# Kernel optimization log

Hardware: AMD Instinct MI355X
Metric: run time of the kernel (lower is better)

## Reference

```python
import jax, jax.numpy as jnp
import numpy as np

N_HEADS = 12

def setup_inputs() -> dict:
    key = jax.random.key(0)
    k1, k2, k3 = jax.random.split(key, 3)
    B, S, W = 8, 1024, 768
    x = jax.random.normal(k1, (B, S, W), dtype=jnp.float32)
    w_qkv = jax.random.normal(k2, (W, 3 * W), dtype=jnp.float32) * (W ** -0.5)
    w_out = jax.random.normal(k3, (W, W), dtype=jnp.float32) * (W ** -0.5)
    return {"x": x, "w_qkv": w_qkv, "w_out": w_out}

def reference(x, w_qkv, w_out):
    B, S, W = x.shape
    H = N_HEADS
    D = W // H  # head_width
    scale = W ** -0.5  # NOTE: source scales by width**-0.5, not head_width**-0.5
    qkv = x @ w_qkv  # [B, S, 3W]
    q, k, v = jnp.split(qkv, 3, axis=2)
    q = q.reshape(B, S, H, D)
    k = k.reshape(B, S, H, D)
    # attn_score: [B, i, j, n]
    attn_score = jnp.einsum('binh,bjnh->bijn', q, k) * scale
    attn_weight = jax.nn.softmax(attn_score, axis=2)
    # NOTE: source uses K (not V) here — faithful reproduction of the bug.
    out = jnp.einsum('bijn,bjnh->binh', attn_weight, k)
    out = out.reshape(B, S, W)
    return out @ w_out  # dropout is identity in eval
```

## Files before the change

kernel.cpp:

```cpp
#include <hip/hip_runtime.h>

#define US unsigned short

typedef __bf16 bf16x8 __attribute__((ext_vector_type(8)));
typedef short s16x8 __attribute__((ext_vector_type(8)));
typedef short s16x4 __attribute__((ext_vector_type(4)));
typedef float f32x4 __attribute__((ext_vector_type(4)));

static __device__ __forceinline__ US f2bf(float f) {
  union { float f; unsigned u; } x; x.f = f;
  unsigned r = x.u + 0x7fffu + ((x.u >> 16) & 1u);
  return (US)(r >> 16);
}

static __device__ __forceinline__ unsigned packbf(float lo, float hi) {
  return (unsigned)f2bf(lo) | ((unsigned)f2bf(hi) << 16);
}

static __device__ __forceinline__ void gload16(const US* g, US* l) {
  __builtin_amdgcn_global_load_lds(
      (const __attribute__((address_space(1))) void*)g,
      (__attribute__((address_space(3))) void*)l, 16, 0, 0);
}

__global__ __launch_bounds__(256) void cast_f32_bf16(
    const float* __restrict__ src, US* __restrict__ dst) {
  int i = blockIdx.x * 256 + threadIdx.x;
  const float4* s = (const float4*)src + (size_t)i * 2;
  float4 a = s[0], b = s[1];
  s16x8 w;
  w[0] = (short)f2bf(a.x); w[1] = (short)f2bf(a.y);
  w[2] = (short)f2bf(a.z); w[3] = (short)f2bf(a.w);
  w[4] = (short)f2bf(b.x); w[5] = (short)f2bf(b.y);
  w[6] = (short)f2bf(b.z); w[7] = (short)f2bf(b.w);
  *(s16x8*)(dst + (size_t)i * 8) = w;
}

__global__ __launch_bounds__(256) void transpose_cast_k(
    const float* __restrict__ src, US* __restrict__ dst, int R, int C,
    float scale, int nlim) {
  __shared__ float t[32][33];
  int n0 = blockIdx.x * 32, r0 = blockIdx.y * 32;
  int tx = threadIdx.x & 31, ty = threadIdx.x >> 5;
  for (int i = 0; i < 4; ++i) {
    int r = i * 8 + ty;
    t[r][tx] = src[(size_t)(r0 + r) * C + n0 + tx];
  }
  __syncthreads();
  for (int i = 0; i < 4; ++i) {
    int n = i * 8 + ty;
    float s = (n0 + n < nlim) ? scale : 1.0f;
    dst[(size_t)(n0 + n) * R + r0 + tx] = f2bf(t[tx][n] * s);
  }
}

__global__ __launch_bounds__(256) void kt_transpose(
    const US* __restrict__ QK, US* __restrict__ KT) {
  __shared__ US t[32][34];
  int bh = blockIdx.z, b = bh / 12, h = bh % 12;
  int s0 = blockIdx.x * 32, d0 = blockIdx.y * 32;
  int tx = threadIdx.x & 31, ty = threadIdx.x >> 5;
  const US* src = QK + ((size_t)b * 1024 + s0) * 1536 + 768 + h * 64 + d0;
  for (int i = 0; i < 4; ++i)
    t[i * 8 + ty][tx] = src[(size_t)(i * 8 + ty) * 1536 + tx];
  __syncthreads();
  US* dst = KT + ((size_t)bh * 64 + d0) * 1024 + s0;
  for (int i = 0; i < 4; ++i)
    dst[(size_t)(i * 8 + ty) * 1024 + tx] = t[tx][i * 8 + ty];
}

template<int OUT_BF16>
__global__ __launch_bounds__(256) void gemm_bt(
    const US* __restrict__ A, const US* __restrict__ Bt,
    void* __restrict__ Cv, int M, int N, int K) {
  __shared__ US As[2][128 * 32];
  __shared__ US Bs[2][128 * 32];
  const int tid = threadIdx.x;
  const int wave = tid >> 6, lane = tid & 63;
  const int lr = lane & 15, lg = lane >> 4;
  const int m0 = blockIdx.x * 128, n0 = blockIdx.y * 128;
  const int wr = (wave >> 1) * 64, wc = (wave & 1) * 64;
  const int srow = tid >> 2;
  const int sseg = (tid & 3) ^ (srow & 3);
  const US* gA = A + (size_t)(m0 + srow) * K + sseg * 8;
  const US* gB = Bt + (size_t)(n0 + srow) * K + sseg * 8;

  f32x4 acc[4][4];
  for (int i = 0; i < 4; ++i)
    for (int j = 0; j < 4; ++j) acc[i][j] = (f32x4){0.f, 0.f, 0.f, 0.f};

  const int nIt = K >> 5;
  for (int i = 0; i < 2; ++i) {
    gload16(gA + (size_t)i * 64 * K, &As[0][tid * 8 + i * 2048]);
    gload16(gB + (size_t)i * 64 * K, &Bs[0][tid * 8 + i * 2048]);
  }
  __syncthreads();

  for (int it = 0; it < nIt; ++it) {
    if (it + 1 < nIt) {
      int k0 = (it + 1) * 32, bb = (it + 1) & 1;
      for (int i = 0; i < 2; ++i) {
        gload16(gA + (size_t)i * 64 * K + k0, &As[bb][tid * 8 + i * 2048]);
        gload16(gB + (size_t)i * 64 * K + k0, &Bs[bb][tid * 8 + i * 2048]);
      }
    }
    const US* Ab = As[it & 1];
    const US* Bb = Bs[it & 1];
    bf16x8 af[4], bfr[4];
    for (int mi = 0; mi < 4; ++mi)
      af[mi] = *(const bf16x8*)(Ab + (wr + mi * 16 + lr) * 32 + ((lg ^ (lr & 3)) * 8));
    for (int ni = 0; ni < 4; ++ni)
      bfr[ni] = *(const bf16x8*)(Bb + (wc + ni * 16 + lr) * 32 + ((lg ^ (lr & 3)) * 8));
    for (int mi = 0; mi < 4; ++mi)
      for (int ni = 0; ni < 4; ++ni)
        acc[mi][ni] = __builtin_amdgcn_mfma_f32_16x16x32_bf16(
            af[mi], bfr[ni], acc[mi][ni], 0, 0, 0);
    __syncthreads();
  }

  for (int mi = 0; mi < 4; ++mi)
    for (int ni = 0; ni < 4; ++ni)
      for (int r = 0; r < 4; ++r) {
        size_t row = (size_t)m0 + wr + mi * 16 + lg * 4 + r;
        size_t col = (size_t)n0 + wc + ni * 16 + lr;
        float v = acc[mi][ni][r];
        if (OUT_BF16) ((US*)Cv)[row * N + col] = f2bf(v);
        else          ((float*)Cv)[row * N + col] = v;
      }
}

__global__ __launch_bounds__(256) void attn_kernel(
    const US* __restrict__ QK, const US* __restrict__ KTg, US* __restrict__ AO) {
  __shared__ US Kr[2][64 * 64];
  __shared__ US Kt[2][64 * 64];
  const int tid = threadIdx.x, wave = tid >> 6, lane = tid & 63;
  const int lr = lane & 15, lg = lane >> 4;
  const int id = blockIdx.y * 16 + blockIdx.x;
  const int bh = (id & 7) * 12 + ((id >> 3) % 12);
  const int qt = id / 96;
  const int b = bh / 12, h = bh % 12;
  const int q0 = qt * 64 + wave * 16;
  const size_t rowbase = (size_t)b * 1024;
  const US* Qp = QK + rowbase * 1536 + h * 64;
  const US* Kp = QK + rowbase * 1536 + 768 + h * 64;
  const US* KTp = KTg + (size_t)bh * 64 * 1024;

  const int srow = tid >> 3;
  const int sseg = (tid & 7) ^ (srow & 7);
  const US* gK = Kp + (size_t)srow * 1536 + sseg * 8;
  const US* gT = KTp + (size_t)srow * 1024 + sseg * 8;

  bf16x8 qf[2];
  for (int kk = 0; kk < 2; ++kk)
    qf[kk] = *(const bf16x8*)(Qp + (size_t)(q0 + lr) * 1536 + kk * 32 + lg * 8);

  const bool odd = (lg & 1) != 0;
  const bool hi = (lg >> 1) != 0;
  const int laneQ0 = lr + 32 * (lg & 1) + 16 * (lg >> 1);
  const int laneQ1 = lr + 32 * (lg & 1) + 16 * (1 - (lg >> 1));

  float lsum = 0.f;
  f32x4 acc[4];
  for (int d = 0; d < 4; ++d) acc[d] = (f32x4){0.f, 0.f, 0.f, 0.f};

  for (int i = 0; i < 2; ++i) {
    gload16(gK + (size_t)(i * 32) * 1536, &Kr[0][tid * 8 + i * 2048]);
    gload16(gT + (size_t)(i * 32) * 1024, &Kt[0][tid * 8 + i * 2048]);
  }
  __syncthreads();

  for (int t = 0; t < 16; ++t) {
    if (t + 1 < 16) {
      int kv0 = (t + 1) * 64, bb = (t + 1) & 1;
      for (int i = 0; i < 2; ++i) {
        gload16(gK + (size_t)(kv0 + i * 32) * 1536, &Kr[bb][tid * 8 + i * 2048]);
        gload16(gT + (size_t)(i * 32) * 1024 + kv0, &Kt[bb][tid * 8 + i * 2048]);
      }
    }
    const US* Krb = Kr[t & 1];
    const US* Ktb = Kt[t & 1];

    f32x4 sv[4];
    __builtin_amdgcn_s_setprio(1);
    for (int ns = 0; ns < 4; ++ns) {
      f32x4 a = {0.f, 0.f, 0.f, 0.f};
      for (int kk = 0; kk < 2; ++kk) {
        bf16x8 kf = *(const bf16x8*)(
            Krb + (ns * 16 + lr) * 64 + (((kk * 4 + lg) ^ (lr & 7)) * 8));
        a = __builtin_amdgcn_mfma_f32_16x16x32_bf16(kf, qf[kk], a, 0, 0, 0);
      }
      sv[ns] = a;
    }
    __builtin_amdgcn_s_setprio(0);

    float p[4][4];
    for (int ns = 0; ns < 4; ++ns)
      for (int r = 0; r < 4; ++r) {
        p[ns][r] = __builtin_amdgcn_exp2f(sv[ns][r]);
        lsum += p[ns][r];
      }
    unsigned pk00 = packbf(p[0][0], p[0][1]), pk01 = packbf(p[0][2], p[0][3]);
    unsigned pk10 = packbf(p[1][0], p[1][1]), pk11 = packbf(p[1][2], p[1][3]);
    unsigned pk20 = packbf(p[2][0], p[2][1]), pk21 = packbf(p[2][2], p[2][3]);
    unsigned pk30 = packbf(p[3][0], p[3][1]), pk31 = packbf(p[3][2], p[3][3]);
    int a0 = (int)(odd ? pk10 : pk00), a1 = (int)(odd ? pk11 : pk01);
    int a2 = (int)(odd ? pk30 : pk20), a3 = (int)(odd ? pk31 : pk21);
    int b0 = (int)(odd ? pk00 : pk10), b1 = (int)(odd ? pk01 : pk11);
    int b2 = (int)(odd ? pk20 : pk30), b3 = (int)(odd ? pk21 : pk31);
    int r0 = __shfl(a0, laneQ0), r1 = __shfl(a1, laneQ0);
    int r2 = __shfl(a2, laneQ0), r3 = __shfl(a3, laneQ0);
    int r4 = __shfl(b0, laneQ1), r5 = __shfl(b1, laneQ1);
    int r6 = __shfl(b2, laneQ1), r7 = __shfl(b3, laneQ1);
    union { unsigned u[4]; bf16x8 v; } pa0, pa1;
    pa0.u[0] = hi ? (unsigned)r4 : (unsigned)r0;
    pa0.u[1] = hi ? (unsigned)r5 : (unsigned)r1;
    pa0.u[2] = hi ? (unsigned)r0 : (unsigned)r4;
    pa0.u[3] = hi ? (unsigned)r1 : (unsigned)r5;
    pa1.u[0] = hi ? (unsigned)r6 : (unsigned)r2;
    pa1.u[1] = hi ? (unsigned)r7 : (unsigned)r3;
    pa1.u[2] = hi ? (unsigned)r2 : (unsigned)r6;
    pa1.u[3] = hi ? (unsigned)r3 : (unsigned)r7;

    __builtin_amdgcn_s_setprio(1);
    for (int d = 0; d < 4; ++d) {
      int drow = d * 16 + lr;
      bf16x8 kf0 = *(const bf16x8*)(Ktb + drow * 64 + ((lg ^ (lr & 7)) * 8));
      acc[d] = __builtin_amdgcn_mfma_f32_16x16x32_bf16(pa0.v, kf0, acc[d], 0, 0, 0);
      bf16x8 kf1 = *(const bf16x8*)(Ktb + drow * 64 + (((4 + lg) ^ (lr & 7)) * 8));
      acc[d] = __builtin_amdgcn_mfma_f32_16x16x32_bf16(pa1.v, kf1, acc[d], 0, 0, 0);
    }
    __builtin_amdgcn_s_setprio(0);
    __syncthreads();
  }

  lsum += __shfl_xor(lsum, 16);
  lsum += __shfl_xor(lsum, 32);
  float inv[4];
  for (int r = 0; r < 4; ++r)
    inv[r] = 1.0f / __shfl(lsum, lg * 4 + r);
  for (int d = 0; d < 4; ++d)
    for (int r = 0; r < 4; ++r) {
      size_t row = rowbase + q0 + lg * 4 + r;
      AO[row * 768 + h * 64 + d * 16 + lr] = f2bf(acc[d][r] * inv[r]);
    }
}

extern "C" void kernel_launch(void* const* d_in, const int* in_sizes, int n_in,
                              void* d_out, int out_size, void* d_ws, size_t ws_size,
                              hipStream_t stream) {
  const float* x    = (const float*)d_in[0];
  const float* wqkv = (const float*)d_in[1];
  const float* wout = (const float*)d_in[2];
  float* out = (float*)d_out;

  US* wqkT  = (US*)d_ws;
  US* woutT = wqkT + (size_t)1536 * 768;
  US* QK    = woutT + (size_t)768 * 768;
  US* AO    = QK + (size_t)8192 * 1536;
  US* xb    = AO + (size_t)8192 * 768;
  US* KT    = xb;

  const float cexp = 0.03608439182435161f * 1.4426950408889634f;

  cast_f32_bf16<<<3072, 256, 0, stream>>>(x, xb);
  transpose_cast_k<<<dim3(48, 24), 256, 0, stream>>>(wqkv, wqkT, 768, 2304, cexp, 768);
  transpose_cast_k<<<dim3(24, 24), 256, 0, stream>>>(wout, woutT, 768, 768, 1.0f, 0);
  gemm_bt<1><<<dim3(64, 12), 256, 0, stream>>>(xb, wqkT, QK, 8192, 1536, 768);
  kt_transpose<<<dim3(32, 2, 96), 256, 0, stream>>>(QK, KT);
  attn_kernel<<<dim3(16, 96), 256, 0, stream>>>(QK, KT, AO);
  gemm_bt<0><<<dim3(64, 6), 256, 0, stream>>>(AO, woutT, out, 8192, 768, 768);
}
```

Measured before the change: 119.4 us.

## Process two query sub-tiles per wave in attention to reuse K fragments

```diff
diff --git a/kernel.cpp b/kernel.cpp
--- a/kernel.cpp
+++ b/kernel.cpp
@@ -129,17 +129,53 @@
       }
 }
 
-__global__ __launch_bounds__(256) void attn_kernel(
+static __device__ __forceinline__ void softmax_route(
+    const f32x4 sv[4], float& lsum, bool odd, bool hi, int laneQ0, int laneQ1,
+    bf16x8& pa0v, bf16x8& pa1v) {
+  float p[4][4];
+#pragma unroll
+  for (int ns = 0; ns < 4; ++ns)
+#pragma unroll
+    for (int r = 0; r < 4; ++r) {
+      p[ns][r] = __builtin_amdgcn_exp2f(sv[ns][r]);
+      lsum += p[ns][r];
+    }
+  unsigned pk00 = packbf(p[0][0], p[0][1]), pk01 = packbf(p[0][2], p[0][3]);
+  unsigned pk10 = packbf(p[1][0], p[1][1]), pk11 = packbf(p[1][2], p[1][3]);
+  unsigned pk20 = packbf(p[2][0], p[2][1]), pk21 = packbf(p[2][2], p[2][3]);
+  unsigned pk30 = packbf(p[3][0], p[3][1]), pk31 = packbf(p[3][2], p[3][3]);
+  int a0 = (int)(odd ? pk10 : pk00), a1 = (int)(odd ? pk11 : pk01);
+  int a2 = (int)(odd ? pk30 : pk20), a3 = (int)(odd ? pk31 : pk21);
+  int b0 = (int)(odd ? pk00 : pk10), b1 = (int)(odd ? pk01 : pk11);
+  int b2 = (int)(odd ? pk20 : pk30), b3 = (int)(odd ? pk21 : pk31);
+  int r0 = __shfl(a0, laneQ0), r1 = __shfl(a1, laneQ0);
+  int r2 = __shfl(a2, laneQ0), r3 = __shfl(a3, laneQ0);
+  int r4 = __shfl(b0, laneQ1), r5 = __shfl(b1, laneQ1);
+  int r6 = __shfl(b2, laneQ1), r7 = __shfl(b3, laneQ1);
+  union { unsigned u[4]; bf16x8 v; } pa0, pa1;
+  pa0.u[0] = hi ? (unsigned)r4 : (unsigned)r0;
+  pa0.u[1] = hi ? (unsigned)r5 : (unsigned)r1;
+  pa0.u[2] = hi ? (unsigned)r0 : (unsigned)r4;
+  pa0.u[3] = hi ? (unsigned)r1 : (unsigned)r5;
+  pa1.u[0] = hi ? (unsigned)r6 : (unsigned)r2;
+  pa1.u[1] = hi ? (unsigned)r7 : (unsigned)r3;
+  pa1.u[2] = hi ? (unsigned)r2 : (unsigned)r6;
+  pa1.u[3] = hi ? (unsigned)r3 : (unsigned)r7;
+  pa0v = pa0.v;
+  pa1v = pa1.v;
+}
+
+__global__ __launch_bounds__(256, 3) void attn_kernel(
     const US* __restrict__ QK, const US* __restrict__ KTg, US* __restrict__ AO) {
   __shared__ US Kr[2][64 * 64];
   __shared__ US Kt[2][64 * 64];
   const int tid = threadIdx.x, wave = tid >> 6, lane = tid & 63;
   const int lr = lane & 15, lg = lane >> 4;
-  const int id = blockIdx.y * 16 + blockIdx.x;
+  const int id = blockIdx.y * 8 + blockIdx.x;
   const int bh = (id & 7) * 12 + ((id >> 3) % 12);
   const int qt = id / 96;
   const int b = bh / 12, h = bh % 12;
-  const int q0 = qt * 64 + wave * 16;
+  const int qw = qt * 128 + wave * 32;
   const size_t rowbase = (size_t)b * 1024;
   const US* Qp = QK + rowbase * 1536 + h * 64;
   const US* Kp = QK + rowbase * 1536 + 768 + h * 64;
@@ -150,18 +186,25 @@
   const US* gK = Kp + (size_t)srow * 1536 + sseg * 8;
   const US* gT = KTp + (size_t)srow * 1024 + sseg * 8;
 
-  bf16x8 qf[2];
-  for (int kk = 0; kk < 2; ++kk)
-    qf[kk] = *(const bf16x8*)(Qp + (size_t)(q0 + lr) * 1536 + kk * 32 + lg * 8);
+  bf16x8 qf0[2], qf1[2];
+#pragma unroll
+  for (int kk = 0; kk < 2; ++kk) {
+    qf0[kk] = *(const bf16x8*)(Qp + (size_t)(qw + lr) * 1536 + kk * 32 + lg * 8);
+    qf1[kk] = *(const bf16x8*)(Qp + (size_t)(qw + 16 + lr) * 1536 + kk * 32 + lg * 8);
+  }
 
   const bool odd = (lg & 1) != 0;
   const bool hi = (lg >> 1) != 0;
   const int laneQ0 = lr + 32 * (lg & 1) + 16 * (lg >> 1);
   const int laneQ1 = lr + 32 * (lg & 1) + 16 * (1 - (lg >> 1));
 
-  float lsum = 0.f;
-  f32x4 acc[4];
-  for (int d = 0; d < 4; ++d) acc[d] = (f32x4){0.f, 0.f, 0.f, 0.f};
+  float lsum0 = 0.f, lsum1 = 0.f;
+  f32x4 acc0[4], acc1[4];
+#pragma unroll
+  for (int d = 0; d < 4; ++d) {
+    acc0[d] = (f32x4){0.f, 0.f, 0.f, 0.f};
+    acc1[d] = (f32x4){0.f, 0.f, 0.f, 0.f};
+  }
 
   for (int i = 0; i < 2; ++i) {
     gload16(gK + (size_t)(i * 32) * 1536, &Kr[0][tid * 8 + i * 2048]);
@@ -180,68 +223,59 @@
     const US* Krb = Kr[t & 1];
     const US* Ktb = Kt[t & 1];
 
-    f32x4 sv[4];
+    f32x4 sv0[4], sv1[4];
     __builtin_amdgcn_s_setprio(1);
+#pragma unroll
     for (int ns = 0; ns < 4; ++ns) {
-      f32x4 a = {0.f, 0.f, 0.f, 0.f};
+      f32x4 a0 = {0.f, 0.f, 0.f, 0.f}, a1 = {0.f, 0.f, 0.f, 0.f};
+#pragma unroll
       for (int kk = 0; kk < 2; ++kk) {
         bf16x8 kf = *(const bf16x8*)(
             Krb + (ns * 16 + lr) * 64 + (((kk * 4 + lg) ^ (lr & 7)) * 8));
-        a = __builtin_amdgcn_mfma_f32_16x16x32_bf16(kf, qf[kk], a, 0, 0, 0);
+        a0 = __builtin_amdgcn_mfma_f32_16x16x32_bf16(kf, qf0[kk], a0, 0, 0, 0);
+        a1 = __builtin_amdgcn_mfma_f32_16x16x32_bf16(kf, qf1[kk], a1, 0, 0, 0);
       }
-      sv[ns] = a;
+      sv0[ns] = a0; sv1[ns] = a1;
     }
     __builtin_amdgcn_s_setprio(0);
 
-    float p[4][4];
-    for (int ns = 0; ns < 4; ++ns)
-      for (int r = 0; r < 4; ++r) {
-        p[ns][r] = __builtin_amdgcn_exp2f(sv[ns][r]);
-        lsum += p[ns][r];
-      }
-    unsigned pk00 = packbf(p[0][0], p[0][1]), pk01 = packbf(p[0][2], p[0][3]);
-    unsigned pk10 = packbf(p[1][0], p[1][1]), pk11 = packbf(p[1][2], p[1][3]);
-    unsigned pk20 = packbf(p[2][0], p[2][1]), pk21 = packbf(p[2][2], p[2][3]);
-    unsigned pk30 = packbf(p[3][0], p[3][1]), pk31 = packbf(p[3][2], p[3][3]);
-    int a0 = (int)(odd ? pk10 : pk00), a1 = (int)(odd ? pk11 : pk01);
-    int a2 = (int)(odd ? pk30 : pk20), a3 = (int)(odd ? pk31 : pk21);
-    int b0 = (int)(odd ? pk00 : pk10), b1 = (int)(odd ? pk01 : pk11);
-    int b2 = (int)(odd ? pk20 : pk30), b3 = (int)(odd ? pk21 : pk31);
-    int r0 = __shfl(a0, laneQ0), r1 = __shfl(a1, laneQ0);
-    int r2 = __shfl(a2, laneQ0), r3 = __shfl(a3, laneQ0);
-    int r4 = __shfl(b0, laneQ1), r5 = __shfl(b1, laneQ1);
-    int r6 = __shfl(b2, laneQ1), r7 = __shfl(b3, laneQ1);
-    union { unsigned u[4]; bf16x8 v; } pa0, pa1;
-    pa0.u[0] = hi ? (unsigned)r4 : (unsigned)r0;
-    pa0.u[1] = hi ? (unsigned)r5 : (unsigned)r1;
-    pa0.u[2] = hi ? (unsigned)r0 : (unsigned)r4;
-    pa0.u[3] = hi ? (unsigned)r1 : (unsigned)r5;
-    pa1.u[0] = hi ? (unsigned)r6 : (unsigned)r2;
-    pa1.u[1] = hi ? (unsigned)r7 : (unsigned)r3;
-    pa1.u[2] = hi ? (unsigned)r2 : (unsigned)r6;
-    pa1.u[3] = hi ? (unsigned)r3 : (unsigned)r7;
+    bf16x8 pa00, pa01, pa10, pa11;
+    softmax_route(sv0, lsum0, odd, hi, laneQ0, laneQ1, pa00, pa01);
+    softmax_route(sv1, lsum1, odd, hi, laneQ0, laneQ1, pa10, pa11);
 
     __builtin_amdgcn_s_setprio(1);
+#pragma unroll
     for (int d = 0; d < 4; ++d) {
       int drow = d * 16 + lr;
       bf16x8 kf0 = *(const bf16x8*)(Ktb + drow * 64 + ((lg ^ (lr & 7)) * 8));
-      acc[d] = __builtin_amdgcn_mfma_f32_16x16x32_bf16(pa0.v, kf0, acc[d], 0, 0, 0);
       bf16x8 kf1 = *(const bf16x8*)(Ktb + drow * 64 + (((4 + lg) ^ (lr & 7)) * 8));
-      acc[d] = __builtin_amdgcn_mfma_f32_16x16x32_bf16(pa1.v, kf1, acc[d], 0, 0, 0);
+      acc0[d] = __builtin_amdgcn_mfma_f32_16x16x32_bf16(pa00, kf0, acc0[d], 0, 0, 0);
+      acc0[d] = __builtin_amdgcn_mfma_f32_16x16x32_bf16(pa01, kf1, acc0[d], 0, 0, 0);
+      acc1[d] = __builtin_amdgcn_mfma_f32_16x16x32_bf16(pa10, kf0, acc1[d], 0, 0, 0);
+      acc1[d] = __builtin_amdgcn_mfma_f32_16x16x32_bf16(pa11, kf1, acc1[d], 0, 0, 0);
     }
     __builtin_amdgcn_s_setprio(0);
     __syncthreads();
   }
 
-  lsum += __shfl_xor(lsum, 16);
-  lsum += __shfl_xor(lsum, 32);
-  float inv[4];
-  for (int r = 0; r < 4; ++r)
-    inv[r] = 1.0f / __shfl(lsum, lg * 4 + r);
+  lsum0 += __shfl_xor(lsum0, 16);
+  lsum0 += __shfl_xor(lsum0, 32);
+  lsum1 += __shfl_xor(lsum1, 16);
+  lsum1 += __shfl_xor(lsum1, 32);
+  float inv0[4], inv1[4];
+#pragma unroll
+  for (int r = 0; r < 4; ++r) {
+    inv0[r] = 1.0f / __shfl(lsum0, lg * 4 + r);
+    inv1[r] = 1.0f / __shfl(lsum1, lg * 4 + r);
+  }
+#pragma unroll
   for (int d = 0; d < 4; ++d)
+#pragma unroll
     for (int r = 0; r < 4; ++r) {
-      size_t row = rowbase + q0 + lg * 4 + r;
-      AO[row * 768 + h * 64 + d * 16 + lr] = f2bf(acc[d][r] * inv[r]);
+      size_t row0 = rowbase + qw + lg * 4 + r;
+      AO[row0 * 768 + h * 64 + d * 16 + lr] = f2bf(acc0[d][r] * inv0[r]);
+      size_t row1 = rowbase + qw + 16 + lg * 4 + r;
+      AO[row1 * 768 + h * 64 + d * 16 + lr] = f2bf(acc1[d][r] * inv1[r]);
     }
 }
 
@@ -267,6 +301,6 @@
   transpose_cast_k<<<dim3(24, 24), 256, 0, stream>>>(wout, woutT, 768, 768, 1.0f, 0);
   gemm_bt<1><<<dim3(64, 12), 256, 0, stream>>>(xb, wqkT, QK, 8192, 1536, 768);
   kt_transpose<<<dim3(32, 2, 96), 256, 0, stream>>>(QK, KT);
-  attn_kernel<<<dim3(16, 96), 256, 0, stream>>>(QK, KT, AO);
+  attn_kernel<<<dim3(8, 96), 256, 0, stream>>>(QK, KT, AO);
   gemm_bt<0><<<dim3(64, 6), 256, 0, stream>>>(AO, woutT, out, 8192, 768, 768);
 }
```

New measurement: 109.3 us. -8.5%, faster.
